# Kernel optimization log

Hardware: AMD Instinct MI355X
Metric: run time of the kernel (lower is better)

Reference implementation:

```python
import jax, jax.numpy as jnp
import numpy as np

B, T, NB = 8192, 18, 6
EH, DH = 256, 256
NIN = NB + 1  # encoder GRU input: bits + feedback scalar


def gru_cell(x, h, Wih, Whh, bih, bhh):
    # PyTorch GRU cell: gates ordered (r, z, n)
    gi = x @ Wih.T + bih
    gh = h @ Whh.T + bhh
    ir, iz, inn = jnp.split(gi, 3, axis=-1)
    hr, hz, hn = jnp.split(gh, 3, axis=-1)
    r = jax.nn.sigmoid(ir + hr)
    z = jax.nn.sigmoid(iz + hz)
    n = jnp.tanh(inn + r * hn)
    return (1.0 - z) * n + z * h


def run_gru_dir(seq, Wih, Whh, bih, bhh, reverse):
    # seq: [T, B, D] -> hidden outputs [T, B, H] (aligned to original time order)
    Bn, H = seq.shape[1], Whh.shape[1]
    def step(h, x):
        h2 = gru_cell(x, h, Wih, Whh, bih, bhh)
        return h2, h2
    _, outs = jax.lax.scan(step, jnp.zeros((Bn, H), seq.dtype), seq, reverse=reverse)
    return outs


def setup_inputs() -> dict:
    key = jax.random.key(0)
    ks = jax.random.split(key, 40)
    def w(k, shape, fan):
        s = 1.0 / np.sqrt(fan)
        return jax.random.uniform(k, shape, jnp.float32, -s, s)
    inp = {}
    inp['b'] = (jax.random.uniform(ks[0], (B, NB)) < 0.5).astype(jnp.float32)
    inp['noise1'] = jax.random.normal(ks[1], (B, T, 1), jnp.float32)
    inp['noise2'] = jax.random.normal(ks[2], (B, T, 1), jnp.float32)
    # encoder GRU (2 layers, unidirectional)
    inp['enc_Wih0'] = w(ks[3], (3 * EH, NIN), EH); inp['enc_Whh0'] = w(ks[4], (3 * EH, EH), EH)
    inp['enc_bih0'] = w(ks[5], (3 * EH,), EH);     inp['enc_bhh0'] = w(ks[6], (3 * EH,), EH)
    inp['enc_Wih1'] = w(ks[7], (3 * EH, EH), EH);  inp['enc_Whh1'] = w(ks[8], (3 * EH, EH), EH)
    inp['enc_bih1'] = w(ks[9], (3 * EH,), EH);     inp['enc_bhh1'] = w(ks[10], (3 * EH,), EH)
    inp['enc_lin_W'] = w(ks[11], (1, EH), EH);     inp['enc_lin_b'] = w(ks[12], (1,), EH)
    inp['weight_power'] = jnp.ones((T,), jnp.float32)
    # decoder GRU (2 layers, bidirectional)
    inp['dec_Wih0f'] = w(ks[13], (3 * DH, 1), DH);      inp['dec_Whh0f'] = w(ks[14], (3 * DH, DH), DH)
    inp['dec_bih0f'] = w(ks[15], (3 * DH,), DH);        inp['dec_bhh0f'] = w(ks[16], (3 * DH,), DH)
    inp['dec_Wih0b'] = w(ks[17], (3 * DH, 1), DH);      inp['dec_Whh0b'] = w(ks[18], (3 * DH, DH), DH)
    inp['dec_bih0b'] = w(ks[19], (3 * DH,), DH);        inp['dec_bhh0b'] = w(ks[20], (3 * DH,), DH)
    inp['dec_Wih1f'] = w(ks[21], (3 * DH, 2 * DH), DH); inp['dec_Whh1f'] = w(ks[22], (3 * DH, DH), DH)
    inp['dec_bih1f'] = w(ks[23], (3 * DH,), DH);        inp['dec_bhh1f'] = w(ks[24], (3 * DH,), DH)
    inp['dec_Wih1b'] = w(ks[25], (3 * DH, 2 * DH), DH); inp['dec_Whh1b'] = w(ks[26], (3 * DH, DH), DH)
    inp['dec_bih1b'] = w(ks[27], (3 * DH,), DH);        inp['dec_bhh1b'] = w(ks[28], (3 * DH,), DH)
    inp['dec_lin_W'] = w(ks[29], (NB, 2 * DH), 2 * DH); inp['dec_lin_b'] = w(ks[30], (NB,), 2 * DH)
    inp['weight_merge'] = jnp.ones((T, 2), jnp.float32)
    return inp


def reference(b, noise1, noise2,
              enc_Wih0, enc_Whh0, enc_bih0, enc_bhh0,
              enc_Wih1, enc_Whh1, enc_bih1, enc_bhh1,
              enc_lin_W, enc_lin_b, weight_power,
              dec_Wih0f, dec_Whh0f, dec_bih0f, dec_bhh0f,
              dec_Wih0b, dec_Whh0b, dec_bih0b, dec_bhh0b,
              dec_Wih1f, dec_Whh1f, dec_bih1f, dec_bhh1f,
              dec_Wih1b, dec_Whh1b, dec_bih1b, dec_bhh1b,
              dec_lin_W, dec_lin_b, weight_merge):
    Bn = b.shape[0]
    Tn = weight_power.shape[0]
    # power-normalized per-step weights: sqrt(w^2 * T / sum(w^2))
    wp = jnp.sqrt(weight_power ** 2 * Tn / jnp.sum(weight_power ** 2))

    def enc_step(carry, xs):
        h0, h1, z = carry
        n1, n2, wpt = xs
        inp = jnp.concatenate([b, z], axis=1)            # [B, NB+1]
        h0n = gru_cell(inp, h0, enc_Wih0, enc_Whh0, enc_bih0, enc_bhh0)
        h1n = gru_cell(h0n, h1, enc_Wih1, enc_Whh1, enc_bih1, enc_bhh1)
        xt = jnp.tanh(h1n @ enc_lin_W.T + enc_lin_b)     # [B, 1]
        xn = (xt - jnp.mean(xt)) / jnp.std(xt, ddof=1)   # training-mode batch norm over whole tensor
        y = xn * wpt + n1                                # received symbol
        return (h0n, h1n, y + n2), y                     # feedback z = y + noise2

    carry0 = (jnp.zeros((Bn, EH), b.dtype), jnp.zeros((Bn, EH), b.dtype), jnp.zeros((Bn, 1), b.dtype))
    xs = (jnp.swapaxes(noise1, 0, 1), jnp.swapaxes(noise2, 0, 1), wp)
    _, y_seq = jax.lax.scan(enc_step, carry0, xs)        # [T, B, 1]

    # bidirectional 2-layer decoder GRU over y
    o0f = run_gru_dir(y_seq, dec_Wih0f, dec_Whh0f, dec_bih0f, dec_bhh0f, False)
    o0b = run_gru_dir(y_seq, dec_Wih0b, dec_Whh0b, dec_bih0b, dec_bhh0b, True)
    s1 = jnp.concatenate([o0f, o0b], axis=-1)            # [T, B, 2*DH]
    o1f = run_gru_dir(s1, dec_Wih1f, dec_Whh1f, dec_bih1f, dec_bhh1f, False)
    o1b = run_gru_dir(s1, dec_Wih1b, dec_Whh1b, dec_bih1b, dec_bhh1b, True)

    # attention_type == 5: learned weighted merge over time, per direction
    wf = jnp.sqrt(weight_merge[:, 0] ** 2 * Tn / jnp.sum(weight_merge[:, 0] ** 2))
    wb = jnp.sqrt(weight_merge[:, 1] ** 2 * Tn / jnp.sum(weight_merge[:, 1] ** 2))
    rf = jnp.einsum('tbh,t->bh', o1f, wf)
    rb = jnp.einsum('tbh,t->bh', o1b, wb)
    rc = jnp.concatenate([rf, rb], axis=1)               # [B, 2*DH]
    out = jax.nn.sigmoid(rc @ dec_lin_W.T + dec_lin_b)   # bit_vector output -> sigmoid
    return out.reshape(Bn, -1, 1)
```

## Files before the change

kernel.cpp:

```cpp
#include <hip/hip_runtime.h>
#include <hip/hip_bf16.h>
#include <math.h>

#define BN_ 8192
#define TT 18
#define NBITS 6
#define HH 256
#define G3 768

typedef __hip_bfloat16 hbf16;
typedef __bf16 bf16x8 __attribute__((ext_vector_type(8)));
typedef float f32x4 __attribute__((ext_vector_type(4)));

__device__ inline float sigm(float x){ return 1.0f/(1.0f + expf(-x)); }
__device__ inline float ldx(const void* p, int i, int bf){
    if(bf){ unsigned short u = ((const unsigned short*)p)[i]; return __uint_as_float(((unsigned)u)<<16); }
    return ((const float*)p)[i];
}
__device__ inline __bf16 f2b(float f){ hbf16 h = __float2bfloat16(f); return *reinterpret_cast<__bf16*>(&h); }
__device__ inline float b2f(__bf16 b){ unsigned short u = *reinterpret_cast<unsigned short*>(&b); return __uint_as_float(((unsigned)u)<<16); }
__device__ inline unsigned pack2(float a, float b){
    hbf16 lo = __float2bfloat16(a), hi = __float2bfloat16(b);
    return (unsigned)*(unsigned short*)&lo | ((unsigned)*(unsigned short*)&hi << 16);
}

__device__ __forceinline__ void gld_lds16(const void* g, void* l){
    __builtin_amdgcn_global_load_lds(
        (const __attribute__((address_space(1))) unsigned int*)g,
        (__attribute__((address_space(3))) unsigned int*)l, 16, 0, 0);
}

__global__ __launch_bounds__(256) void fillz(float* __restrict__ p, int n){
    for(int i = blockIdx.x*256 + threadIdx.x; i < n; i += gridDim.x*256) p[i] = 0.0f;
}
__global__ __launch_bounds__(256) void fillb(__bf16* __restrict__ p, int n){
    for(int i = blockIdx.x*256 + threadIdx.x; i < n; i += gridDim.x*256) p[i] = f2b(0.0f);
}

__global__ void prep_w(const void* wp, const void* wm, unsigned* flag,
                       float* wpn, float* wfn, float* wbn){
    if(threadIdx.x==0 && blockIdx.x==0){
        unsigned w0 = *(const unsigned*)wp;
        int bf = ((w0 >> 16) == (w0 & 0xFFFFu)) ? 1 : 0;
        flag[0] = (unsigned)bf;
        float s=0; for(int t=0;t<TT;t++){ float v=ldx(wp,t,bf); s += v*v; }
        for(int t=0;t<TT;t++){ float v=ldx(wp,t,bf); wpn[t] = sqrtf(v*v*TT/s); }
        float sf=0, sb=0;
        for(int t=0;t<TT;t++){ float f=ldx(wm,2*t,bf), b=ldx(wm,2*t+1,bf); sf += f*f; sb += b*b; }
        for(int t=0;t<TT;t++){
            float f=ldx(wm,2*t,bf), b=ldx(wm,2*t+1,bf);
            wfn[t] = sqrtf(f*f*TT/sf);
            wbn[t] = sqrtf(b*b*TT/sb);
        }
    }
}

struct CJ { const void* src; void* dst; int n; int K; int mode; };
struct CJs { CJ j[20]; };
__global__ __launch_bounds__(256) void conv_all(CJs J, const unsigned* __restrict__ flagp){
    const int bf = (int)*flagp;
    CJ c = J.j[blockIdx.y];
    for(int i = blockIdx.x*256 + threadIdx.x; i < c.n; i += gridDim.x*256){
        if(c.mode==1){
            int row = i / c.K, k = i - row*c.K;
            int g = row>>8, jj = row&255;
            int prow = ((jj>>4)*48) + g*16 + (jj&15);
            ((__bf16*)c.dst)[(size_t)prow*c.K + k] = f2b(ldx(c.src, i, bf));
        }else if(c.mode==2){
            int t = i >> 13, b = i & (BN_-1);
            ((float*)c.dst)[i] = ldx(c.src, b*TT + t, bf);
        }else{
            ((float*)c.dst)[i] = ldx(c.src, i, bf);
        }
    }
}

struct FQ {
    const __bf16* A1; const __bf16* W1; int K1;
    const __bf16* A2; const __bf16* W2; int K2;
    const float* bgi; const float* bgh;
    const __bf16* h; __bf16* hout;
    const void* bits; const void* wih0raw; const void* bih0raw; const float* zf;
    const void* linw; float* xt;
    const float* y; const void* wihraw; const void* bihraw; __bf16* s1t;
    float* racc; const float* wct;
};
struct FQ2 { FQ q[2]; };

template<int MODE>
__global__ __launch_bounds__(256,3) void fused_step(FQ2 PP, const unsigned* __restrict__ flagp){
    const FQ P = PP.q[blockIdx.z];
    const int bf = (int)*flagp;
    __shared__ __align__(16) char smem[28672];
    __bf16* As = (__bf16*)smem;
    __bf16* Ws = (__bf16*)(smem + 16384);
    float*  T  = (float*)smem;
    const int tid = threadIdx.x;
    const int mt = blockIdx.x*8 + (blockIdx.y>>3);
    const int jt = blockIdx.y & 7;
    const int m0 = mt*128;
    const int n0 = jt*96;
    const int lane = tid&63, wv = tid>>6;
    const int wvbase = tid & ~63;
    const int wrow = wv>>1, wcol = wv&1;
    const int q = lane>>4, n15 = lane&15;

    f32x4 accR[4], accZ[4], accN1[4], accN2[4];
    #pragma unroll
    for(int i=0;i<4;i++){ accR[i]=(f32x4){0,0,0,0}; accZ[i]=(f32x4){0,0,0,0};
                          accN1[i]=(f32x4){0,0,0,0}; accN2[i]=(f32x4){0,0,0,0}; }

    #pragma unroll
    for(int ph = 0; ph < 2; ph++){
        if(ph==0 && !(MODE==1 || MODE==3)) continue;
        const __bf16* __restrict__ A = ph ? P.A2 : P.A1;
        const __bf16* __restrict__ W = ph ? P.W2 : P.W1;
        const int K = ph ? P.K2 : P.K1;
        for(int k0=0;k0<K;k0+=64){
            #pragma unroll
            for(int s=0;s<4;s++){
                int c = tid + 256*s;
                int row = c>>3, slot = c&7;
                int qc = slot ^ ((row>>1)&7);
                gld_lds16(A + (size_t)(m0+row)*K + k0 + qc*8,
                          smem + (s*256 + wvbase)*16);
            }
            #pragma unroll
            for(int s=0;s<3;s++){
                int c = tid + 256*s;
                int row = c>>3, slot = c&7;
                int qc = slot ^ ((row>>1)&7);
                gld_lds16(W + (size_t)(n0+row)*K + k0 + qc*8,
                          smem + 16384 + (s*256 + wvbase)*16);
            }
            __syncthreads();
            #pragma unroll
            for(int ks=0;ks<2;ks++){
                const int cq = ks*4 + q;
                bf16x8 af[4], bfr[3];
                #pragma unroll
                for(int i=0;i<4;i++){
                    int R = wrow*64+i*16+n15;
                    int col = cq ^ ((R>>1)&7);
                    af[i] = *(const bf16x8*)&As[R*64 + col*8];
                }
                #pragma unroll
                for(int g=0;g<3;g++){
                    int RW = wcol*48+g*16+n15;
                    int col = cq ^ ((RW>>1)&7);
                    bfr[g] = *(const bf16x8*)&Ws[RW*64 + col*8];
                }
                #pragma unroll
                for(int i=0;i<4;i++){
                    accR[i] = __builtin_amdgcn_mfma_f32_16x16x32_bf16(af[i], bfr[0], accR[i], 0,0,0);
                    accZ[i] = __builtin_amdgcn_mfma_f32_16x16x32_bf16(af[i], bfr[1], accZ[i], 0,0,0);
                    if(ph) accN2[i] = __builtin_amdgcn_mfma_f32_16x16x32_bf16(af[i], bfr[2], accN2[i], 0,0,0);
                    else   accN1[i] = __builtin_amdgcn_mfma_f32_16x16x32_bf16(af[i], bfr[2], accN1[i], 0,0,0);
                }
            }
            __syncthreads();
        }
    }

    const int jl = wcol*16 + n15;
    const int j  = jt*32 + jl;
    const float bghr = P.bgh[j], bghz = P.bgh[256+j], bghn = P.bgh[512+j];
    float bgir=0, bgiz=0, bgin=0;
    if(MODE==1 || MODE==3){ bgir = P.bgi[j]; bgiz = P.bgi[256+j]; bgin = P.bgi[512+j]; }
    float w0r[7], w0z[7], w0n[7];
    if(MODE==0){
        #pragma unroll
        for(int k=0;k<7;k++){
            w0r[k] = ldx(P.wih0raw, (j    )*7+k, bf);
            w0z[k] = ldx(P.wih0raw, (j+256)*7+k, bf);
            w0n[k] = ldx(P.wih0raw, (j+512)*7+k, bf);
        }
        bgir = ldx(P.bih0raw, j, bf); bgiz = ldx(P.bih0raw, j+256, bf); bgin = ldx(P.bih0raw, j+512, bf);
    }
    float wy_r=0, wy_z=0, wy_n=0;
    if(MODE==2){
        wy_r = ldx(P.wihraw, j, bf); wy_z = ldx(P.wihraw, j+256, bf); wy_n = ldx(P.wihraw, j+512, bf);
        bgir = ldx(P.bihraw, j, bf); bgiz = ldx(P.bihraw, j+256, bf); bgin = ldx(P.bihraw, j+512, bf);
    }
    const float linwj = (MODE==1) ? ldx(P.linw, j, bf) : 0.0f;
    const float wct   = (MODE==3) ? P.wct[0] : 0.0f;

    #pragma unroll
    for(int i=0;i<4;i++){
        const int rbl = wrow*64 + i*16 + q*4;
        float vred[4];
        #pragma unroll
        for(int r=0;r<4;r++){
            const int row_l = rbl + r;
            const int row = m0 + row_l;
            float gir, giz, gin;
            if(MODE==1 || MODE==3){
                gir = bgir; giz = bgiz; gin = accN1[i][r] + bgin;
            }else if(MODE==0){
                gir = bgir; giz = bgiz; gin = bgin;
                #pragma unroll
                for(int k=0;k<NBITS;k++){
                    float bv = ldx(P.bits, row*NBITS+k, bf);
                    gir += bv*w0r[k]; giz += bv*w0z[k]; gin += bv*w0n[k];
                }
                float zb = P.zf[row];
                gir += zb*w0r[6]; giz += zb*w0z[6]; gin += zb*w0n[6];
            }else{
                float yv = P.y[row];
                gir = yv*wy_r + bgir; giz = yv*wy_z + bgiz; gin = yv*wy_n + bgin;
            }
            float rr = sigm(gir + accR[i][r] + bghr);
            float zz = sigm(giz + accZ[i][r] + bghz);
            float nn = tanhf(gin + rr*(accN2[i][r] + bghn));
            float hold = b2f(P.h[(size_t)row*HH + j]);
            float hn = (1.0f - zz)*nn + zz*hold;
            T[row_l*33 + jl] = hn;
            if(MODE==1) vred[r] = hn*linwj;
        }
        if(MODE==1){
            #pragma unroll
            for(int r=0;r<4;r++){
                float v = vred[r];
                #pragma unroll
                for(int m=1;m<16;m<<=1) v += __shfl_xor(v, m);
                if(n15==0) atomicAdd(&P.xt[m0+rbl+r], v);
            }
        }
    }
    __syncthreads();

    const int rw2 = tid>>2, cw = tid&3;
    #pragma unroll
    for(int pass=0; pass<2; pass++){
        const int row_l = pass*64 + rw2;
        const int row = m0 + row_l;
        float v[8];
        #pragma unroll
        for(int u=0;u<8;u++) v[u] = T[row_l*33 + cw*8 + u];
        uint4 pkv = { pack2(v[0],v[1]), pack2(v[2],v[3]), pack2(v[4],v[5]), pack2(v[6],v[7]) };
        *(uint4*)&P.hout[(size_t)row*HH + jt*32 + cw*8] = pkv;
        if(MODE==2) *(uint4*)&P.s1t[(size_t)row*512 + jt*32 + cw*8] = pkv;
        if(MODE==3){
            float* rp = &P.racc[(size_t)row*HH + jt*32 + cw*8];
            float4 a0 = *(float4*)rp, a1 = *(float4*)(rp+4);
            a0.x += wct*v[0]; a0.y += wct*v[1]; a0.z += wct*v[2]; a0.w += wct*v[3];
            a1.x += wct*v[4]; a1.y += wct*v[5]; a1.z += wct*v[6]; a1.w += wct*v[7];
            *(float4*)rp = a0; *(float4*)(rp+4) = a1;
        }
    }
}

__global__ __launch_bounds__(1024) void stats_emit(float* __restrict__ xt, const void* __restrict__ lb,
        const float* __restrict__ wpn, int t, const float* __restrict__ n1t, const float* __restrict__ n2t,
        float* __restrict__ yseq, float* __restrict__ zf, const unsigned* __restrict__ flagp){
    const int bf = (int)*flagp;
    const float lbv = ldx(lb, 0, bf);
    int tid = threadIdx.x;
    float s=0.0f, ss=0.0f;
    for(int i=tid;i<BN_;i+=1024){ float v = tanhf(xt[i] + lbv); s += v; ss += v*v; }
    #pragma unroll
    for(int o=32;o;o>>=1){ s += __shfl_down(s,o); ss += __shfl_down(ss,o); }
    __shared__ float S[16], SS[16], stm[2];
    if((tid&63)==0){ S[tid>>6]=s; SS[tid>>6]=ss; }
    __syncthreads();
    if(tid==0){
        float a=0.0f, b=0.0f;
        for(int i=0;i<16;i++){ a+=S[i]; b+=SS[i]; }
        float mean = a/(float)BN_;
        float var = (b - (float)BN_*mean*mean)/(float)(BN_-1);
        stm[0]=mean; stm[1]=1.0f/sqrtf(var);
    }
    __syncthreads();
    const float mean=stm[0], rs=stm[1], wt=wpn[t];
    for(int i=tid;i<BN_;i+=1024){
        float v = tanhf(xt[i] + lbv);
        float y = (v-mean)*rs*wt + n1t[i];
        yseq[(size_t)t*BN_ + i] = y;
        zf[i] = y + n2t[i];
        xt[i] = 0.0f;
    }
}

__global__ __launch_bounds__(256) void final_k(const float* __restrict__ rf, const float* __restrict__ rb,
        const void* __restrict__ W, const void* __restrict__ bias, void* __restrict__ out,
        const unsigned* __restrict__ flagp){
    const int bf = (int)*flagp;
    int lane = threadIdx.x & 63;
    int row = blockIdx.x*4 + (threadIdx.x>>6);
    float a[6] = {};
    #pragma unroll
    for(int i=0;i<4;i++){
        int c = lane + 64*i;
        float xf = rf[(size_t)row*HH + c];
        float xb = rb[(size_t)row*HH + c];
        #pragma unroll
        for(int k=0;k<6;k++) a[k] += xf*ldx(W, k*512 + c, bf) + xb*ldx(W, k*512 + 256 + c, bf);
    }
    #pragma unroll
    for(int o=32;o;o>>=1){
        #pragma unroll
        for(int k=0;k<6;k++) a[k] += __shfl_down(a[k], o);
    }
    if(lane==0){
        #pragma unroll
        for(int k=0;k<6;k++){
            float v = sigm(a[k] + ldx(bias,k,bf));
            if(bf) ((hbf16*)out)[(size_t)row*6+k] = __float2bfloat16(v);
            else   ((float*)out)[(size_t)row*6+k] = v;
        }
    }
}

extern "C" void kernel_launch(void* const* d_in, const int* in_sizes, int n_in,
                              void* d_out, int out_size, void* d_ws, size_t ws_size,
                              hipStream_t stream)
{
    (void)in_sizes; (void)n_in; (void)out_size;
    const void* bits  = d_in[0];
    const void* n1    = d_in[1];
    const void* n2    = d_in[2];
    const void* eWih0 = d_in[3];
    const void* eWhh0 = d_in[4];
    const void* ebih0 = d_in[5];
    const void* ebhh0 = d_in[6];
    const void* eWih1 = d_in[7];
    const void* eWhh1 = d_in[8];
    const void* ebih1 = d_in[9];
    const void* ebhh1 = d_in[10];
    const void* elinW = d_in[11];
    const void* elinb = d_in[12];
    const void* wpow  = d_in[13];
    const void* dWih0f= d_in[14];
    const void* dWhh0f= d_in[15];
    const void* dbih0f= d_in[16];
    const void* dbhh0f= d_in[17];
    const void* dWih0b= d_in[18];
    const void* dWhh0b= d_in[19];
    const void* dbih0b= d_in[20];
    const void* dbhh0b= d_in[21];
    const void* dWih1f= d_in[22];
    const void* dWhh1f= d_in[23];
    const void* dbih1f= d_in[24];
    const void* dbhh1f= d_in[25];
    const void* dWih1b= d_in[26];
    const void* dWhh1b= d_in[27];
    const void* dbih1b= d_in[28];
    const void* dbhh1b= d_in[29];
    const void* dlinW = d_in[30];
    const void* dlinb = d_in[31];
    const void* wmrg  = d_in[32];

    float* base = (float*)d_ws;
    size_t off = 0;
    auto alloc  = [&](size_t n){ float* p = base + off; off += (n + 63) & ~(size_t)63; return p; };
    auto allocb = [&](size_t n){ __bf16* p = (__bf16*)(base + off); off += ((n/2) + 63) & ~(size_t)63; return p; };
    unsigned* flag = (unsigned*)alloc(64);
    float* wpn = alloc(TT); float* wfn = alloc(TT); float* wbn = alloc(TT);
    const int WK = HH*G3;
    __bf16* WeHH0 = allocb(WK);  __bf16* WeIH1 = allocb(WK);  __bf16* WeHH1 = allocb(WK);
    __bf16* Wd0f  = allocb(WK);  __bf16* Wd0b  = allocb(WK);
    __bf16* Wd1fI = allocb(2*WK);__bf16* Wd1bI = allocb(2*WK);
    __bf16* Wd1fH = allocb(WK);  __bf16* Wd1bH = allocb(WK);
    float* BeHH0 = alloc(G3); float* BeIH1 = alloc(G3); float* BeHH1 = alloc(G3);
    float* Bd0f  = alloc(G3); float* Bd0b  = alloc(G3);
    float* Bd1fI = alloc(G3); float* Bd1bI = alloc(G3);
    float* Bd1fH = alloc(G3); float* Bd1bH = alloc(G3);
    const size_t NH = (size_t)BN_*HH;
    __bf16* X0 = allocb(NH);  __bf16* X1 = allocb(NH);
    __bf16* Y0 = allocb(NH);  __bf16* Y1 = allocb(NH);
    float* rf  = alloc(NH);
    float* rb  = alloc(NH);
    float* xt  = alloc(BN_);
    float* zf  = alloc(BN_);
    float* yseq= alloc((size_t)TT*BN_);
    float* n1t = alloc((size_t)TT*BN_);
    float* n2t = alloc((size_t)TT*BN_);
    __bf16* s1 = allocb((size_t)TT*BN_*512);
    size_t need = off*sizeof(float);
    if(ws_size < need) return;

    prep_w<<<1,64,0,stream>>>(wpow, wmrg, flag, wpn, wfn, wbn);
    CJs J;
    const void* ws_src[20] = {eWhh0,eWih1,eWhh1,dWhh0f,dWhh0b,dWih1f,dWih1b,dWhh1f,dWhh1b,
                              ebhh0,ebih1,ebhh1,dbhh0f,dbhh0b,dbih1f,dbih1b,dbhh1f,dbhh1b, n1, n2};
    void* ws_dst[20] = {WeHH0,WeIH1,WeHH1,Wd0f,Wd0b,Wd1fI,Wd1bI,Wd1fH,Wd1bH,
                        BeHH0,BeIH1,BeHH1,Bd0f,Bd0b,Bd1fI,Bd1bI,Bd1fH,Bd1bH, n1t, n2t};
    int ws_n[20] = {WK,WK,WK,WK,WK,2*WK,2*WK,WK,WK, G3,G3,G3,G3,G3,G3,G3,G3,G3, TT*BN_, TT*BN_};
    int ws_K[20] = {256,256,256,256,256,512,512,256,256, 0,0,0,0,0,0,0,0,0, 0,0};
    int ws_m[20] = {1,1,1,1,1,1,1,1,1, 0,0,0,0,0,0,0,0,0, 2,2};
    for(int i=0;i<20;i++){ J.j[i] = {ws_src[i], ws_dst[i], ws_n[i], ws_K[i], ws_m[i]}; }
    conv_all<<<dim3(768,20),256,0,stream>>>(J, flag);
    fillb<<<1024,256,0,stream>>>(X0, (int)NH);
    fillb<<<1024,256,0,stream>>>(Y0, (int)NH);
    fillz<<<32,256,0,stream>>>(xt, BN_);
    fillz<<<32,256,0,stream>>>(zf, BN_);

    dim3 g1(8, 64, 1), g2(8, 64, 2);
    __bf16* X[2] = {X0, X1};
    __bf16* Y[2] = {Y0, Y1};

    int p = 0;
    for(int t=0;t<TT;t++){
        FQ2 P0{}; FQ2 P1{};
        FQ& a = P0.q[0];
        a.A2=X[p]; a.W2=WeHH0; a.K2=HH; a.bgh=BeHH0; a.h=X[p]; a.hout=X[1-p];
        a.bits=bits; a.wih0raw=eWih0; a.bih0raw=ebih0; a.zf=zf;
        fused_step<0><<<g1,256,0,stream>>>(P0, flag);
        FQ& b = P1.q[0];
        b.A1=X[1-p]; b.W1=WeIH1; b.K1=HH; b.A2=Y[p]; b.W2=WeHH1; b.K2=HH;
        b.bgi=BeIH1; b.bgh=BeHH1; b.h=Y[p]; b.hout=Y[1-p];
        b.linw=elinW; b.xt=xt;
        fused_step<1><<<g1,256,0,stream>>>(P1, flag);
        stats_emit<<<1,1024,0,stream>>>(xt, elinb, wpn, t, n1t+(size_t)t*BN_, n2t+(size_t)t*BN_,
                                        yseq, zf, flag);
        p ^= 1;
    }

    fillb<<<1024,256,0,stream>>>(X0, (int)NH);
    fillb<<<1024,256,0,stream>>>(Y0, (int)NH);
    p = 0;
    for(int i=0;i<TT;i++){
        int tf = i, tb = TT-1-i;
        FQ2 P{};
        FQ& a = P.q[0];
        a.A2=X[p]; a.W2=Wd0f; a.K2=HH; a.bgh=Bd0f; a.h=X[p]; a.hout=X[1-p];
        a.y=yseq+(size_t)tf*BN_; a.wihraw=dWih0f; a.bihraw=dbih0f; a.s1t=s1+(size_t)tf*BN_*512;
        FQ& b = P.q[1];
        b.A2=Y[p]; b.W2=Wd0b; b.K2=HH; b.bgh=Bd0b; b.h=Y[p]; b.hout=Y[1-p];
        b.y=yseq+(size_t)tb*BN_; b.wihraw=dWih0b; b.bihraw=dbih0b; b.s1t=s1+(size_t)tb*BN_*512+256;
        fused_step<2><<<g2,256,0,stream>>>(P, flag);
        p ^= 1;
    }

    fillb<<<1024,256,0,stream>>>(X0, (int)NH);
    fillb<<<1024,256,0,stream>>>(Y0, (int)NH);
    fillz<<<1024,256,0,stream>>>(rf, (int)(2*NH));
    p = 0;
    for(int i=0;i<TT;i++){
        int tf = i, tb = TT-1-i;
        FQ2 P{};
        FQ& a = P.q[0];
        a.A1=s1+(size_t)tf*BN_*512; a.W1=Wd1fI; a.K1=512;
        a.A2=X[p]; a.W2=Wd1fH; a.K2=HH; a.bgi=Bd1fI; a.bgh=Bd1fH; a.h=X[p]; a.hout=X[1-p];
        a.racc=rf; a.wct=wfn+tf;
        FQ& b = P.q[1];
        b.A1=s1+(size_t)tb*BN_*512; b.W1=Wd1bI; b.K1=512;
        b.A2=Y[p]; b.W2=Wd1bH; b.K2=HH; b.bgi=Bd1bI; b.bgh=Bd1bH; b.h=Y[p]; b.hout=Y[1-p];
        b.racc=rb; b.wct=wbn+tb;
        fused_step<3><<<g2,256,0,stream>>>(P, flag);
        p ^= 1;
    }

    final_k<<<BN_/4,256,0,stream>>>(rf, rb, dlinW, dlinb, d_out, flag);
}
```

Measured before the change: 1.782 ms.

## Fuse encoder feedback stats into GRU step and fold decoder head into layer-1 steps

Replaces the per-timestep single-block stats_emit launch with a redundant per-block batch reduction inside the next encoder layer-0 step, using double-buffered xt accumulators. The decoder's final linear projection is pushed into each layer-1 step as a per-tile partial dot product with dlinW, so the large fp32 rf/rb accumulators, their zero fill and read-modify-write traffic disappear. A small out_head kernel then sums the 16 partials. The trade-off is that every block recomputes an 8192-element tanh reduction, and the extra work is added to the epilogue.

```diff
diff --git a/kernel.cpp b/kernel.cpp
--- a/kernel.cpp
+++ b/kernel.cpp
@@ -80,7 +80,7 @@
     const __bf16* A2; const __bf16* W2; int K2;
     const float* bgi; const float* bgh;
     const __bf16* h; __bf16* hout;
-    const void* bits; const void* wih0raw; const void* bih0raw; const float* zf;
+    const void* bits; const void* wih0raw; const void* bih0raw;
     const void* linw; float* xt;
     const float* y; const void* wihraw; const void* bihraw; __bf16* s1t;
     float* racc; const float* wct;
@@ -92,6 +92,8 @@
     const FQ P = PP.q[blockIdx.z];
     const int bf = (int)*flagp;
     __shared__ __align__(16) char smem[28672];
+    __shared__ float zs[192];
+    __shared__ float sred[4], ssred[4];
     __bf16* As = (__bf16*)smem;
     __bf16* Ws = (__bf16*)(smem + 16384);
     float*  T  = (float*)smem;
@@ -104,6 +106,40 @@
     const int wvbase = tid & ~63;
     const int wrow = wv>>1, wcol = wv&1;
     const int q = lane>>4, n15 = lane&15;
+
+    if(MODE==0){
+        if(P.K1){
+            const float lbv = ldx(P.linw, 0, bf);
+            const float wt  = P.wct[0];
+            const float* __restrict__ xr = P.xt;
+            float s=0.0f, ss=0.0f;
+            const float4* x4 = (const float4*)xr;
+            for(int i=tid;i<BN_/4;i+=256){
+                float4 vv = x4[i];
+                float a0=tanhf(vv.x+lbv), a1=tanhf(vv.y+lbv), a2=tanhf(vv.z+lbv), a3=tanhf(vv.w+lbv);
+                s += a0+a1+a2+a3; ss += a0*a0+a1*a1+a2*a2+a3*a3;
+            }
+            #pragma unroll
+            for(int o=32;o;o>>=1){ s += __shfl_xor(s,o); ss += __shfl_xor(ss,o); }
+            if(lane==0){ sred[wv]=s; ssred[wv]=ss; }
+            __syncthreads();
+            float a = sred[0]+sred[1]+sred[2]+sred[3];
+            float bq = ssred[0]+ssred[1]+ssred[2]+ssred[3];
+            float mean = a/(float)BN_;
+            float var = (bq - (float)BN_*mean*mean)/(float)(BN_-1);
+            float rs = 1.0f/sqrtf(var);
+            if(tid<128){
+                int row = m0 + tid;
+                float v = tanhf(xr[row]+lbv);
+                float yv = (v-mean)*rs*wt + P.y[row];
+                zs[tid] = yv + ((const float*)P.wihraw)[row];
+                if(jt==0){ ((float*)P.s1t)[row] = yv; P.racc[row] = 0.0f; }
+            }
+        }else{
+            if(tid<128) zs[tid] = 0.0f;
+        }
+        __syncthreads();
+    }
 
     f32x4 accR[4], accZ[4], accN1[4], accN2[4];
     #pragma unroll
@@ -183,7 +219,6 @@
         bgir = ldx(P.bihraw, j, bf); bgiz = ldx(P.bihraw, j+256, bf); bgin = ldx(P.bihraw, j+512, bf);
     }
     const float linwj = (MODE==1) ? ldx(P.linw, j, bf) : 0.0f;
-    const float wct   = (MODE==3) ? P.wct[0] : 0.0f;
 
     #pragma unroll
     for(int i=0;i<4;i++){
@@ -203,7 +238,7 @@
                     float bv = ldx(P.bits, row*NBITS+k, bf);
                     gir += bv*w0r[k]; giz += bv*w0z[k]; gin += bv*w0n[k];
                 }
-                float zb = P.zf[row];
+                float zb = zs[row_l];
                 gir += zb*w0r[6]; giz += zb*w0z[6]; gin += zb*w0n[6];
             }else{
                 float yv = P.y[row];
@@ -226,6 +261,10 @@
                 if(n15==0) atomicAdd(&P.xt[m0+rbl+r], v);
             }
         }
+    }
+    if(MODE==3 && tid<192){
+        int k = tid>>5, jj = tid&31;
+        zs[tid] = ldx(P.bits, k*512 + (int)blockIdx.z*256 + jt*32 + jj, bf);
     }
     __syncthreads();
 
@@ -240,12 +279,19 @@
         uint4 pkv = { pack2(v[0],v[1]), pack2(v[2],v[3]), pack2(v[4],v[5]), pack2(v[6],v[7]) };
         *(uint4*)&P.hout[(size_t)row*HH + jt*32 + cw*8] = pkv;
         if(MODE==2) *(uint4*)&P.s1t[(size_t)row*512 + jt*32 + cw*8] = pkv;
-        if(MODE==3){
-            float* rp = &P.racc[(size_t)row*HH + jt*32 + cw*8];
-            float4 a0 = *(float4*)rp, a1 = *(float4*)(rp+4);
-            a0.x += wct*v[0]; a0.y += wct*v[1]; a0.z += wct*v[2]; a0.w += wct*v[3];
-            a1.x += wct*v[4]; a1.y += wct*v[5]; a1.z += wct*v[6]; a1.w += wct*v[7];
-            *(float4*)rp = a0; *(float4*)(rp+4) = a1;
+    }
+    if(MODE==3){
+        float* pp = P.xt + (size_t)(jt + 8*(int)blockIdx.z)*(BN_*NBITS);
+        const float wct3 = P.wct[0];
+        #pragma unroll
+        for(int u=0;u<3;u++){
+            int idx = tid + 256*u;
+            int row_l = idx/6, k = idx - row_l*6;
+            float dot = 0.0f;
+            #pragma unroll
+            for(int jj=0;jj<32;jj++) dot += T[row_l*33+jj]*zs[k*32+jj];
+            size_t gi = (size_t)(m0+row_l)*NBITS + k;
+            pp[gi] += wct3*dot;
         }
     }
 }
@@ -281,34 +327,18 @@
     }
 }
 
-__global__ __launch_bounds__(256) void final_k(const float* __restrict__ rf, const float* __restrict__ rb,
-        const void* __restrict__ W, const void* __restrict__ bias, void* __restrict__ out,
-        const unsigned* __restrict__ flagp){
+__global__ __launch_bounds__(256) void out_head(const float* __restrict__ pp, const void* __restrict__ bias,
+        void* __restrict__ out, const unsigned* __restrict__ flagp){
     const int bf = (int)*flagp;
-    int lane = threadIdx.x & 63;
-    int row = blockIdx.x*4 + (threadIdx.x>>6);
-    float a[6] = {};
-    #pragma unroll
-    for(int i=0;i<4;i++){
-        int c = lane + 64*i;
-        float xf = rf[(size_t)row*HH + c];
-        float xb = rb[(size_t)row*HH + c];
-        #pragma unroll
-        for(int k=0;k<6;k++) a[k] += xf*ldx(W, k*512 + c, bf) + xb*ldx(W, k*512 + 256 + c, bf);
-    }
-    #pragma unroll
-    for(int o=32;o;o>>=1){
-        #pragma unroll
-        for(int k=0;k<6;k++) a[k] += __shfl_down(a[k], o);
-    }
-    if(lane==0){
-        #pragma unroll
-        for(int k=0;k<6;k++){
-            float v = sigm(a[k] + ldx(bias,k,bf));
-            if(bf) ((hbf16*)out)[(size_t)row*6+k] = __float2bfloat16(v);
-            else   ((float*)out)[(size_t)row*6+k] = v;
-        }
-    }
+    int i = blockIdx.x*256 + threadIdx.x;
+    if(i >= BN_*NBITS) return;
+    float s = 0.0f;
+    #pragma unroll
+    for(int k=0;k<16;k++) s += pp[(size_t)k*(BN_*NBITS) + i];
+    int kk = i - (i/6)*6;
+    float v = sigm(s + ldx(bias, kk, bf));
+    if(bf) ((hbf16*)out)[i] = __float2bfloat16(v);
+    else   ((float*)out)[i] = v;
 }
 
 extern "C" void kernel_launch(void* const* d_in, const int* in_sizes, int n_in,
@@ -368,9 +398,9 @@
     const size_t NH = (size_t)BN_*HH;
     __bf16* X0 = allocb(NH);  __bf16* X1 = allocb(NH);
     __bf16* Y0 = allocb(NH);  __bf16* Y1 = allocb(NH);
-    float* rf  = alloc(NH);
-    float* rb  = alloc(NH);
-    float* xt  = alloc(BN_);
+    float* pout = alloc((size_t)16*BN_*NBITS);
+    float* xtA = alloc(BN_);
+    float* xtB = alloc(BN_);
     float* zf  = alloc(BN_);
     float* yseq= alloc((size_t)TT*BN_);
     float* n1t = alloc((size_t)TT*BN_);
@@ -392,29 +422,41 @@
     conv_all<<<dim3(768,20),256,0,stream>>>(J, flag);
     fillb<<<1024,256,0,stream>>>(X0, (int)NH);
     fillb<<<1024,256,0,stream>>>(Y0, (int)NH);
-    fillz<<<32,256,0,stream>>>(xt, BN_);
-    fillz<<<32,256,0,stream>>>(zf, BN_);
+    fillz<<<32,256,0,stream>>>(xtA, BN_);
+    fillz<<<32,256,0,stream>>>(xtB, BN_);
+    fillz<<<192,256,0,stream>>>(pout, 16*BN_*NBITS);
 
     dim3 g1(8, 64, 1), g2(8, 64, 2);
     __bf16* X[2] = {X0, X1};
     __bf16* Y[2] = {Y0, Y1};
+    float* xts[2] = {xtA, xtB};
 
     int p = 0;
     for(int t=0;t<TT;t++){
         FQ2 P0{}; FQ2 P1{};
         FQ& a = P0.q[0];
         a.A2=X[p]; a.W2=WeHH0; a.K2=HH; a.bgh=BeHH0; a.h=X[p]; a.hout=X[1-p];
-        a.bits=bits; a.wih0raw=eWih0; a.bih0raw=ebih0; a.zf=zf;
+        a.bits=bits; a.wih0raw=eWih0; a.bih0raw=ebih0;
+        a.K1 = (t>0) ? 1 : 0;
+        if(t>0){
+            a.xt   = xts[(t-1)&1];
+            a.racc = xts[t&1];
+            a.y    = n1t + (size_t)(t-1)*BN_;
+            a.wihraw = (const void*)(n2t + (size_t)(t-1)*BN_);
+            a.s1t  = (__bf16*)(yseq + (size_t)(t-1)*BN_);
+            a.wct  = wpn + (t-1);
+            a.linw = elinb;
+        }
         fused_step<0><<<g1,256,0,stream>>>(P0, flag);
         FQ& b = P1.q[0];
         b.A1=X[1-p]; b.W1=WeIH1; b.K1=HH; b.A2=Y[p]; b.W2=WeHH1; b.K2=HH;
         b.bgi=BeIH1; b.bgh=BeHH1; b.h=Y[p]; b.hout=Y[1-p];
-        b.linw=elinW; b.xt=xt;
+        b.linw=elinW; b.xt=xts[t&1];
         fused_step<1><<<g1,256,0,stream>>>(P1, flag);
-        stats_emit<<<1,1024,0,stream>>>(xt, elinb, wpn, t, n1t+(size_t)t*BN_, n2t+(size_t)t*BN_,
-                                        yseq, zf, flag);
         p ^= 1;
     }
+    stats_emit<<<1,1024,0,stream>>>(xts[(TT-1)&1], elinb, wpn, TT-1,
+                                    n1t+(size_t)(TT-1)*BN_, n2t+(size_t)(TT-1)*BN_, yseq, zf, flag);
 
     fillb<<<1024,256,0,stream>>>(X0, (int)NH);
     fillb<<<1024,256,0,stream>>>(Y0, (int)NH);
@@ -434,7 +476,6 @@
 
     fillb<<<1024,256,0,stream>>>(X0, (int)NH);
     fillb<<<1024,256,0,stream>>>(Y0, (int)NH);
-    fillz<<<1024,256,0,stream>>>(rf, (int)(2*NH));
     p = 0;
     for(int i=0;i<TT;i++){
         int tf = i, tb = TT-1-i;
@@ -442,14 +483,14 @@
         FQ& a = P.q[0];
         a.A1=s1+(size_t)tf*BN_*512; a.W1=Wd1fI; a.K1=512;
         a.A2=X[p]; a.W2=Wd1fH; a.K2=HH; a.bgi=Bd1fI; a.bgh=Bd1fH; a.h=X[p]; a.hout=X[1-p];
-        a.racc=rf; a.wct=wfn+tf;
+        a.bits=dlinW; a.xt=pout; a.wct=wfn+tf;
         FQ& b = P.q[1];
         b.A1=s1+(size_t)tb*BN_*512; b.W1=Wd1bI; b.K1=512;
         b.A2=Y[p]; b.W2=Wd1bH; b.K2=HH; b.bgi=Bd1bI; b.bgh=Bd1bH; b.h=Y[p]; b.hout=Y[1-p];
-        b.racc=rb; b.wct=wbn+tb;
+        b.bits=dlinW; b.xt=pout; b.wct=wbn+tb;
         fused_step<3><<<g2,256,0,stream>>>(P, flag);
         p ^= 1;
     }
 
-    final_k<<<BN_/4,256,0,stream>>>(rf, rb, dlinW, dlinb, d_out, flag);
-}
+    out_head<<<192,256,0,stream>>>(pout, dlinb, d_out, flag);
+}
```

Result: no change. 1.791 ms (+0.5%).
